# Performance work log

Hardware: AMD Instinct MI355X
Metric: run time of the kernel (lower is better)

## Reference

```python
import jax, jax.numpy as jnp
import numpy as np

N_STATE = 32  # SSM states per channel (S4D)


def lrelu(x):
    return jnp.where(x >= 0, x, 0.3 * x)


def conv1d(x, w, b, stride=1, pad=0, dil=1):
    # x: [B,C,L], w: [O,I,K]
    y = jax.lax.conv_general_dilated(
        x, w, (stride,), [(pad, pad)], rhs_dilation=(dil,),
        dimension_numbers=('NCH', 'OIH', 'NCH'))
    return y + b[None, :, None]


def batchnorm(x, g, b, eps=1e-5):
    # training-mode BatchNorm1d: stats over (B, L) per channel
    m = jnp.mean(x, axis=(0, 2), keepdims=True)
    v = jnp.var(x, axis=(0, 2), keepdims=True)
    return (x - m) * jax.lax.rsqrt(v + eps) * g[None, :, None] + b[None, :, None]


def s4_layer(u, log_dt, C2, D):
    # Diagonal S4 (S4D-Lin): u [B,H,L] -> y [B,H,L]; causal FFT conv + skip
    H, N = C2.shape[0], C2.shape[1]
    L = u.shape[-1]
    A = -0.5 + 1j * jnp.pi * jnp.arange(N, dtype=jnp.float32)            # [N]
    dtA = jnp.exp(log_dt)[:, None] * A[None, :]                          # [H,N]
    C = (C2[..., 0] + 1j * C2[..., 1]) * (jnp.exp(dtA) - 1.0) / A        # [H,N]
    vand = jnp.exp(dtA[:, :, None] * jnp.arange(L, dtype=jnp.float32))   # [H,N,L]
    K = 2.0 * jnp.real(jnp.einsum('hn,hnl->hl', C, vand))                # [H,L]
    uf = jnp.fft.rfft(u, n=2 * L)
    Kf = jnp.fft.rfft(K, n=2 * L)
    y = jnp.fft.irfft(uf * Kf[None], n=2 * L)[..., :L]
    return y + D[None, :, None] * u


def down_block(x, s4p, convs, g, b):
    # dilated residual inception down block: S4 then 4 stride-4 dilated convs
    x = s4_layer(x, *s4p)
    d1 = batchnorm(conv1d(x, convs[0][0], convs[0][1], 4, 1, 1), g, b)
    d2 = batchnorm(lrelu(conv1d(x, convs[1][0], convs[1][1], 4, 2, 2)), g, b)
    d3 = batchnorm(lrelu(conv1d(x, convs[2][0], convs[2][1], 4, 4, 4)), g, b)
    d4 = batchnorm(lrelu(conv1d(x, convs[3][0], convs[3][1], 4, 8, 8)), g, b)
    return jnp.concatenate([d1, d2, d3, d4], axis=1)


def setup_inputs() -> dict:
    key = jax.random.key(0)
    ks = iter(jax.random.split(key, 64))

    def nrm(shape, scale=1.0):
        return jax.random.normal(next(ks), shape, jnp.float32) * scale

    def logdt(H):
        lo, hi = np.log(0.001), np.log(0.1)
        return jax.random.uniform(next(ks), (H,), jnp.float32) * (hi - lo) + lo

    B, L, DIN = 16, 8192, 2
    inp = {}
    inp['x'] = nrm((B, L, DIN))
    inp['enc_w'] = nrm((64, DIN, 1), (1.0 / DIN) ** 0.5)
    inp['enc_b'] = jnp.zeros((64,), jnp.float32)
    for pfx, H in (('s4a', 64), ('s4b', 256), ('s4c', 1024)):
        inp[pfx + '_log_dt'] = logdt(H)
        inp[pfx + '_C'] = nrm((H, N_STATE, 2), 0.5 ** 0.5)
        inp[pfx + '_D'] = nrm((H,))
    for blk, C in (('b1', 64), ('b2', 256)):
        sc = (1.0 / (C * 3)) ** 0.5
        for i in range(1, 5):
            inp[f'{blk}_w{i}'] = nrm((C, C, 3), sc)
            inp[f'{blk}_b{i}'] = nrm((C,), 0.02)
    inp['bn1_g'] = jnp.ones((64,), jnp.float32)
    inp['bn1_b'] = jnp.zeros((64,), jnp.float32)
    inp['bn2_g'] = jnp.ones((256,), jnp.float32)
    inp['bn2_b'] = jnp.zeros((256,), jnp.float32)
    inp['dec1_w'] = nrm((256, 1024, 1), (1.0 / 1024) ** 0.5)
    inp['dec1_b'] = jnp.zeros((256,), jnp.float32)
    inp['dec2_w'] = nrm((1, 256, 1), (1.0 / 256) ** 0.5)
    inp['dec2_b'] = jnp.zeros((1,), jnp.float32)
    return inp


def reference(x, enc_w, enc_b,
              s4a_log_dt, s4a_C, s4a_D,
              b1_w1, b1_b1, b1_w2, b1_b2, b1_w3, b1_b3, b1_w4, b1_b4, bn1_g, bn1_b,
              s4b_log_dt, s4b_C, s4b_D,
              b2_w1, b2_b1, b2_w2, b2_b2, b2_w3, b2_b3, b2_w4, b2_b4, bn2_g, bn2_b,
              s4c_log_dt, s4c_C, s4c_D,
              dec1_w, dec1_b, dec2_w, dec2_b):
    h = conv1d(jnp.transpose(x, (0, 2, 1)), enc_w, enc_b)                 # [B,64,L]
    x1 = down_block(h, (s4a_log_dt, s4a_C, s4a_D),
                    [(b1_w1, b1_b1), (b1_w2, b1_b2), (b1_w3, b1_b3), (b1_w4, b1_b4)],
                    bn1_g, bn1_b)                                          # [B,256,L/4]
    x2 = down_block(x1, (s4b_log_dt, s4b_C, s4b_D),
                    [(b2_w1, b2_b1), (b2_w2, b2_b2), (b2_w3, b2_b3), (b2_w4, b2_b4)],
                    bn2_g, bn2_b)                                          # [B,1024,L/16]
    x3 = s4_layer(x2, s4c_log_dt, s4c_C, s4c_D)
    y = conv1d(conv1d(x3, dec1_w, dec1_b), dec2_w, dec2_b)                 # [B,1,L/16]
    ff = jnp.squeeze(y, axis=1)                                            # [B,L/16]
    return ff[..., -1:]                                                    # [B,1]
```

## Files before the change

### kernel.cpp

```cpp
#include <hip/hip_runtime.h>
#include <math.h>

#define PI_F 3.14159265358979323846f

typedef __attribute__((ext_vector_type(8))) short short8;
typedef __attribute__((ext_vector_type(4))) float f32x4;

__device__ __forceinline__ unsigned short f2bf(float f) {
    unsigned int u = __float_as_uint(f);
    unsigned int r = (u + 0x7fffu + ((u >> 16) & 1u)) >> 16;
    return (unsigned short)r;
}
__device__ __forceinline__ float bf2f(unsigned short v) {
    return __uint_as_float((unsigned int)v << 16);
}

__global__ __launch_bounds__(256) void enc_kernel(
    const float* __restrict__ x, const float* __restrict__ ew,
    const float* __restrict__ eb, unsigned short* __restrict__ u1)
{
    int idx = blockIdx.x * 256 + threadIdx.x;
    int t4 = idx & 2047;
    int b  = (idx >> 11) & 15;
    int h  = idx >> 15;
    float w0 = ew[2*h], w1 = ew[2*h+1], bb = eb[h];
    const float* xp = x + ((size_t)b*8192 + (size_t)t4*4)*2;
    float4 a = *(const float4*)xp;
    float4 c = *(const float4*)(xp + 4);
    ushort4 o;
    o.x = f2bf(fmaf(w0, a.x, fmaf(w1, a.y, bb)));
    o.y = f2bf(fmaf(w0, a.z, fmaf(w1, a.w, bb)));
    o.z = f2bf(fmaf(w0, c.x, fmaf(w1, c.y, bb)));
    o.w = f2bf(fmaf(w0, c.z, fmaf(w1, c.w, bb)));
    *(ushort4*)(u1 + ((size_t)h*16 + b)*8192 + (size_t)t4*4) = o;
}

__global__ __launch_bounds__(256) void prep_w(
    const float* __restrict__ w0, const float* __restrict__ w1,
    const float* __restrict__ w2, const float* __restrict__ w3,
    const float* __restrict__ w4, const float* __restrict__ w5,
    const float* __restrict__ w6, const float* __restrict__ w7,
    unsigned short* __restrict__ wprep)
{
    int id = blockIdx.y;
    const float* src; int Cin; size_t doff;
    switch (id) {
        case 0: src = w0; Cin = 64;  doff = 0;      break;
        case 1: src = w1; Cin = 64;  doff = 12288;  break;
        case 2: src = w2; Cin = 64;  doff = 24576;  break;
        case 3: src = w3; Cin = 64;  doff = 36864;  break;
        case 4: src = w4; Cin = 256; doff = 49152;  break;
        case 5: src = w5; Cin = 256; doff = 245760; break;
        case 6: src = w6; Cin = 256; doff = 442368; break;
        default: src = w7; Cin = 256; doff = 638976; break;
    }
    int e = blockIdx.x * 256 + threadIdx.x;
    if (e >= Cin * Cin * 3) return;
    int kb  = e / (Cin * 32);
    int rem = e - kb * (Cin * 32);
    int o   = rem >> 5;
    int kk  = rem & 31;
    int cch = kb / 6, t6 = kb % 6, k = t6 >> 1, chalf = t6 & 1;
    int c = cch * 64 + chalf * 32 + kk;
    wprep[doff + e] = f2bf(src[((size_t)o * Cin + c) * 3 + k]);
}

__global__ __launch_bounds__(128) void prep_s4(
    const float* __restrict__ log_dt, const float* __restrict__ C2,
    const float* __restrict__ Dv,
    unsigned short* __restrict__ TA, unsigned short* __restrict__ VA,
    float* __restrict__ rs, float* __restrict__ Vrs)
{
    int h = blockIdx.x, t = threadIdx.x;
    __shared__ float cn[64];
    __shared__ float sK[128];
    __shared__ unsigned short s_w[128 * 66];
    float dt = expf(log_dt[h]);
    if (t < 32) {
        int n = t;
        float e = expf(-0.5f*dt);
        float s_, c_; sincosf(PI_F*dt*n, &s_, &c_);
        float wr = e*c_, wi = e*s_;
        float ar = -0.5f, ai = PI_F*n;
        float den = 1.f/(ar*ar + ai*ai);
        float tr = wr - 1.f, ti = wi;
        float qr = (tr*ar + ti*ai)*den;
        float qi = (ti*ar - tr*ai)*den;
        float c2r = C2[((size_t)h*32+n)*2], c2i = C2[((size_t)h*32+n)*2+1];
        cn[2*n]   = 2.f*(c2r*qr - c2i*qi);
        cn[2*n+1] = 2.f*(c2r*qi + c2i*qr);
        float e128 = expf(-64.f*dt);
        float s2, c2v; sincosf(PI_F*dt*n*128.f, &s2, &c2v);
        float pr = 1.f - e128*c2v, pim = -e128*s2;
        float dr = 1.f - wr, di = -wi;
        float dd = 1.f/(dr*dr + di*di);
        Vrs[(size_t)h*64 + 2*n]   = (pr*dr + pim*di)*dd;
        Vrs[(size_t)h*64 + 2*n+1] = (pim*dr - pr*di)*dd;
    }
    __syncthreads();
    {
        float em = expf(-0.5f*dt*t);
        float Kt = 0.f;
        for (int n = 0; n < 32; n++) {
            float s_, c_; sincosf(PI_F*dt*(float)(n*t), &s_, &c_);
            Kt += cn[2*n]*em*c_ - cn[2*n+1]*em*s_;
        }
        sK[t] = Kt + (t == 0 ? Dv[h] : 0.f);
    }
    if (t < 64) {
        int n = t >> 1, ri = t & 1;
        float e = expf(-0.5f*dt);
        float s_, c_; sincosf(PI_F*dt*n, &s_, &c_);
        float wr = e*c_, wi = e*s_;
        float crn = cn[2*n], cin = cn[2*n+1];
        float pr = wr, pim = wi;
        for (int m = 0; m < 128; m++) {
            float re = crn*pr - cin*pim;
            float im = crn*pim + cin*pr;
            s_w[m*66 + t] = f2bf(ri ? -im : re);
            float nr = pr*wr - pim*wi;
            float ni = pr*wi + pim*wr;
            pr = nr; pim = ni;
        }
    } else {
        int r = t - 64; int n = r >> 1, ri = r & 1;
        float e = expf(-0.5f*dt);
        float s_, c_; sincosf(PI_F*dt*n, &s_, &c_);
        float wr = e*c_, wi = e*s_;
        float cr2 = 1.f, ci2 = 0.f;
        for (int kb = 3; kb >= 0; kb--) {
            unsigned short buf[32];
            for (int kk = 31; kk >= 0; kk--) {
                buf[kk] = f2bf(ri ? ci2 : cr2);
                float nr = cr2*wr - ci2*wi;
                float ni = cr2*wi + ci2*wr;
                cr2 = nr; ci2 = ni;
            }
            uint4* dst = (uint4*)&VA[(((size_t)h*4 + kb)*64 + r)*32];
            uint4* src = (uint4*)buf;
            dst[0]=src[0]; dst[1]=src[1]; dst[2]=src[2]; dst[3]=src[3];
        }
    }
    __syncthreads();
    {
        float acc = 0.f;
        for (int tau = 0; tau <= t; tau++) acc += sK[tau];
        rs[(size_t)h*128 + t] = acc;
    }
    for (int kb = 0; kb < 4; kb++) {
        unsigned short tb[32];
#pragma unroll
        for (int kk = 0; kk < 32; kk++) {
            int col = kb*32 + kk;
            tb[kk] = f2bf((col <= t) ? sK[t - col] : 0.f);
        }
        uint4* dst = (uint4*)&TA[(((size_t)h*6 + kb)*128 + t)*32];
        uint4* src = (uint4*)tb;
        dst[0]=src[0]; dst[1]=src[1]; dst[2]=src[2]; dst[3]=src[3];
    }
    for (int i = t; i < 1024; i += 128) {
        int kb = i >> 9;
        int rem = i & 511;
        int m = rem >> 2, kkg = rem & 3;
        *(uint4*)&TA[(((size_t)h*6 + 4 + kb)*128 + m)*32 + kkg*8] =
            *(const uint4*)&s_w[m*66 + kb*32 + kkg*8];
    }
}

template<int NCH, int LOGNCH>
__global__ __launch_bounds__(64) void s4ab_fused(
    const unsigned short* __restrict__ u, const unsigned short* __restrict__ VA,
    const float* __restrict__ Vrs, const float* __restrict__ sc,
    const float* __restrict__ sh, const float* __restrict__ log_dt,
    unsigned short* __restrict__ Sini)
{
    const int L = NCH * 128;
    __shared__ float sE[NCH * 68];
    int b = blockIdx.x, h = blockIdx.y;
    int lane = threadIdx.x;
    int nl = lane & 15, g = lane >> 4;
    float scv = sc ? sc[h] : 1.f;
    float shv = sh ? sh[h] : 0.f;

#pragma unroll
    for (int cg = 0; cg < NCH/16; cg++) {
        int c = cg*16 + nl;
        const unsigned short* up = u + ((size_t)h*16 + b)*L + c*128;
        f32x4 acc[4];
#pragma unroll
        for (int mt = 0; mt < 4; mt++) acc[mt] = (f32x4){0.f,0.f,0.f,0.f};
#pragma unroll
        for (int kb = 0; kb < 4; kb++) {
            short8 bf = *(const short8*)(up + kb*32 + g*8);
#pragma unroll
            for (int mt = 0; mt < 4; mt++) {
                short8 af = *(const short8*)(VA + (((size_t)h*4 + kb)*64 + mt*16 + nl)*32 + g*8);
                acc[mt] = __builtin_amdgcn_mfma_f32_16x16x32_bf16(af, bf, acc[mt], 0, 0, 0);
            }
        }
#pragma unroll
        for (int mt = 0; mt < 4; mt++) {
            int j0 = mt*16 + g*4;
            float4 vr = *(const float4*)(Vrs + (size_t)h*64 + j0);
            sE[c*68 + j0 + 0] = fmaf(scv, acc[mt][0], shv*vr.x);
            sE[c*68 + j0 + 1] = fmaf(scv, acc[mt][1], shv*vr.y);
            sE[c*68 + j0 + 2] = fmaf(scv, acc[mt][2], shv*vr.z);
            sE[c*68 + j0 + 3] = fmaf(scv, acc[mt][3], shv*vr.w);
        }
    }
    __syncthreads();
    if (lane < 32) {
        int n = lane;
        float dt = expf(log_dt[h]);
        float e = expf(-0.5f * dt);
        float s_, c_; sincosf(PI_F * dt * n, &s_, &c_);
        float Wr = e*c_, Wi = e*s_;
#pragma unroll
        for (int i = 0; i < 7; i++) { float r = Wr*Wr - Wi*Wi; float im = 2.f*Wr*Wi; Wr = r; Wi = im; }
        float Sr = 0.f, Si = 0.f;
        for (int c2 = 0; c2 < NCH; c2++) {
            float* ep = &sE[c2*68 + 2*n];
            float er = ep[0], ei = ep[1];
            ep[0] = Sr; ep[1] = Si;
            float r  = fmaf(Wr, Sr, fmaf(-Wi, Si, er));
            float im = fmaf(Wi, Sr, fmaf( Wr, Si, ei));
            Sr = r; Si = im;
        }
    }
    __syncthreads();
    unsigned short* sp = Sini + ((size_t)h*16 + b)*NCH*64;
    for (int i = lane*4; i < NCH*64; i += 256) {
        int c2 = i >> 6, j = i & 63;
        ushort4 q;
        q.x = f2bf(sE[c2*68 + j]);
        q.y = f2bf(sE[c2*68 + j+1]);
        q.z = f2bf(sE[c2*68 + j+2]);
        q.w = f2bf(sE[c2*68 + j+3]);
        *(ushort4*)&sp[i] = q;
    }
}

template<int NCH, int LOGNCH>
__global__ __launch_bounds__(256) void s4_gemm_c(
    const unsigned short* __restrict__ u, const unsigned short* __restrict__ Sini,
    const unsigned short* __restrict__ TA, const float* __restrict__ rs,
    const float* __restrict__ sc, const float* __restrict__ sh,
    unsigned short* __restrict__ yout)
{
    const int L = NCH * 128;
    __shared__ unsigned short s_u[64*200];
    __shared__ unsigned short s_s[64*72];
    int h = blockIdx.y;
    int tid = threadIdx.x;
    int lane = tid & 63, wid = tid >> 6;
    int nl = lane & 15, g = lane >> 4;
    int col0 = blockIdx.x * 64;
    for (int i = tid; i < 1024; i += 256) {
        int cl = i >> 4, o = i & 15;
        int col = col0 + cl; int b = col >> LOGNCH, c = col & (NCH - 1);
        *(uint4*)&s_u[cl*200 + o*8] =
            *(const uint4*)&u[((size_t)h*16 + b)*L + c*128 + o*8];
    }
    for (int i = tid; i < 1024; i += 256) {
        int cl = i >> 4, o = i & 15;
        int col = col0 + cl; int b = col >> LOGNCH, c = col & (NCH - 1);
        *(ushort4*)&s_s[cl*72 + o*4] =
            *(const ushort4*)&Sini[(((size_t)h*16 + b)*NCH + c)*64 + o*4];
    }
    __syncthreads();
    f32x4 accT[2][4], accW[2][4];
#pragma unroll
    for (int a = 0; a < 2; a++)
#pragma unroll
        for (int j = 0; j < 4; j++) { accT[a][j] = (f32x4){0,0,0,0}; accW[a][j] = (f32x4){0,0,0,0}; }
#pragma unroll
    for (int kb = 0; kb < 4; kb++) {
        short8 bfr[4];
#pragma unroll
        for (int j = 0; j < 4; j++)
            bfr[j] = *(const short8*)&s_u[(j*16 + nl)*200 + kb*32 + g*8];
#pragma unroll
        for (int mt2 = 0; mt2 < 2; mt2++) {
            int mtile = wid*2 + mt2;
            short8 af = *(const short8*)&TA[(((size_t)h*6 + kb)*128 + mtile*16 + nl)*32 + g*8];
#pragma unroll
            for (int j = 0; j < 4; j++)
                accT[mt2][j] = __builtin_amdgcn_mfma_f32_16x16x32_bf16(af, bfr[j], accT[mt2][j], 0, 0, 0);
        }
    }
#pragma unroll
    for (int kw = 0; kw < 2; kw++) {
        short8 bfr[4];
#pragma unroll
        for (int j = 0; j < 4; j++)
            bfr[j] = *(const short8*)&s_s[(j*16 + nl)*72 + kw*32 + g*8];
#pragma unroll
        for (int mt2 = 0; mt2 < 2; mt2++) {
            int mtile = wid*2 + mt2;
            short8 af = *(const short8*)&TA[(((size_t)h*6 + 4 + kw)*128 + mtile*16 + nl)*32 + g*8];
#pragma unroll
            for (int j = 0; j < 4; j++)
                accW[mt2][j] = __builtin_amdgcn_mfma_f32_16x16x32_bf16(af, bfr[j], accW[mt2][j], 0, 0, 0);
        }
    }
    float scv = sc ? sc[h] : 1.f;
    float shv = sh ? sh[h] : 0.f;
#pragma unroll
    for (int mt2 = 0; mt2 < 2; mt2++) {
        int m0 = (wid*2 + mt2)*16 + g*4;
        float4 rsv = *(const float4*)&rs[(size_t)h*128 + m0];
#pragma unroll
        for (int j = 0; j < 4; j++) {
            int col = col0 + j*16 + nl; int b = col >> LOGNCH, c = col & (NCH - 1);
            ushort4 q;
            q.x = f2bf(fmaf(scv, accT[mt2][j][0], shv*rsv.x) + accW[mt2][j][0]);
            q.y = f2bf(fmaf(scv, accT[mt2][j][1], shv*rsv.y) + accW[mt2][j][1]);
            q.z = f2bf(fmaf(scv, accT[mt2][j][2], shv*rsv.z) + accW[mt2][j][2]);
            q.w = f2bf(fmaf(scv, accT[mt2][j][3], shv*rsv.w) + accW[mt2][j][3]);
            *(ushort4*)&yout[((size_t)h*16 + b)*L + c*128 + m0] = q;
        }
    }
}

template<int CIN, int TBLK>
__global__ __launch_bounds__(256, 2) void conv_mfma4(
    const unsigned short* __restrict__ u, const unsigned short* __restrict__ wp,
    const float* __restrict__ bs0, const float* __restrict__ bs1,
    const float* __restrict__ bs2, const float* __restrict__ bs3,
    unsigned short* __restrict__ out, int Lin, int Lout)
{
    constexpr int F     = TBLK / 16;
    constexpr int NPOS  = TBLK * 4 + 16;
    constexpr int Q     = NPOS / 4;
    constexpr int NITEM = (NPOS / 8) * 64;
    constexpr int NLD   = (NITEM + 255) / 256;
    constexpr int NCC   = CIN / 64;
    constexpr int NBUF  = (NCC > 1) ? 2 : 1;
    constexpr int BUFSZ = 4 * Q * 64;
    __shared__ unsigned short s_in[NBUF * BUFSZ];

    int tid = threadIdx.x;
    int lane = tid & 63, wid = tid >> 6;
    int nl = lane & 15, g = lane >> 4;
    int t0 = blockIdx.x * TBLK;
    int b  = blockIdx.y;
    int og = blockIdx.z * 64;
    const int P0 = t0 * 4 - 8;
    const int DIL = 1 << wid;

    f32x4 acc[4][F];
#pragma unroll
    for (int m = 0; m < 4; m++)
#pragma unroll
        for (int f = 0; f < F; f++) acc[m][f] = (f32x4){0.f,0.f,0.f,0.f};

    uint4 stg[NLD];

    auto stage_load = [&](int ccbase) {
#pragma unroll
        for (int j = 0; j < NLD; j++) {
            int i = tid + 256 * j;
            uint4 v; v.x = 0u; v.y = 0u; v.z = 0u; v.w = 0u;
            if (i < NITEM) {
                int ch = i & 63, po = i >> 6;
                int p = P0 + po * 8;
                const unsigned short* gp = u + ((size_t)(ccbase + ch)*16 + b)*Lin;
                if (p >= 0 && p + 8 <= Lin) {
                    v = *(const uint4*)(gp + p);
                } else {
                    alignas(16) unsigned short t8[8];
#pragma unroll
                    for (int j2 = 0; j2 < 8; j2++) {
                        int pj = p + j2;
                        t8[j2] = ((unsigned)pj < (unsigned)Lin) ? gp[pj] : (unsigned short)0;
                    }
                    v = *(const uint4*)t8;
                }
            }
            stg[j] = v;
        }
    };
    auto stage_write = [&](int bufidx) {
        unsigned short* sb = s_in + bufidx * BUFSZ;
#pragma unroll
        for (int j = 0; j < NLD; j++) {
            int i = tid + 256 * j;
            if (i < NITEM) {
                int ch = i & 63, po = i >> 6;
                alignas(16) unsigned short t8[8];
                *(uint4*)t8 = stg[j];
#pragma unroll
                for (int jj = 0; jj < 8; jj++) {
                    int pl = po * 8 + jj;
                    int row = (pl & 3) * Q + (pl >> 2);
                    sb[row * 64 + (ch ^ ((row & 7) << 3))] = t8[jj];
                }
            }
        }
    };

    stage_load(0);
    stage_write(0);
    __syncthreads();

#pragma unroll
    for (int cc = 0; cc < NCC; cc++) {
        if (cc + 1 < NCC) stage_load((cc + 1) * 64);
        const unsigned short* sb = s_in + (NBUF > 1 ? (cc & 1) * BUFSZ : 0);
#pragma unroll
        for (int k = 0; k < 3; ++k) {
            const int off = (k - 1) * DIL + 8;
            const int r = off & 3, s = off >> 2;
#pragma unroll
            for (int chalf = 0; chalf < 2; ++chalf) {
                int kb = cc * 6 + k * 2 + chalf;
                short8 bfr[F];
#pragma unroll
                for (int f = 0; f < F; ++f) {
                    int q = f*16 + nl + s;
                    int row = r * Q + q;
                    bfr[f] = *(const short8*)&sb[row * 64 +
                        ((((chalf << 2) | g) ^ (row & 7)) << 3)];
                }
#pragma unroll
                for (int m = 0; m < 4; ++m) {
                    short8 afrag = *(const short8*)&wp[(size_t)wid*(3*CIN*CIN) +
                        ((size_t)kb*CIN + og + m*16 + nl)*32 + g*8];
#pragma unroll
                    for (int f = 0; f < F; ++f)
                        acc[m][f] = __builtin_amdgcn_mfma_f32_16x16x32_bf16(afrag, bfr[f], acc[m][f], 0, 0, 0);
                }
            }
        }
        if (cc + 1 < NCC) {
            __syncthreads();
            stage_write((cc + 1) & 1);
            __syncthreads();
        }
    }

    const float* bp = (wid == 0) ? bs0 : (wid == 1) ? bs1 : (wid == 2) ? bs2 : bs3;
#pragma unroll
    for (int m = 0; m < 4; ++m) {
#pragma unroll
        for (int f = 0; f < F; ++f) {
            int t = t0 + f*16 + nl;
#pragma unroll
            for (int r2 = 0; r2 < 4; ++r2) {
                int o = og + m*16 + g*4 + r2;
                float v = acc[m][f][r2] + bp[o];
                if (wid) v = v >= 0.f ? v : 0.3f*v;
                out[((size_t)(wid*CIN + o)*16 + b)*Lout + t] = f2bf(v);
            }
        }
    }
}

__global__ __launch_bounds__(256) void bn_stats(
    const unsigned short* __restrict__ x, const float* __restrict__ g,
    const float* __restrict__ bb, float* __restrict__ sc, float* __restrict__ sh,
    int n, int gmask)
{
    int ch = blockIdx.x;
    const unsigned short* xp = x + (size_t)ch * n;
    float s1 = 0.f, s2 = 0.f;
    for (int i = threadIdx.x*8; i < n; i += 2048) {
        uint4 raw = *(const uint4*)(xp + i);
        unsigned short us[8]; *(uint4*)us = raw;
#pragma unroll
        for (int j = 0; j < 8; j++) {
            float v = bf2f(us[j]);
            s1 += v; s2 += v*v;
        }
    }
    for (int o = 32; o > 0; o >>= 1) { s1 += __shfl_down(s1, o); s2 += __shfl_down(s2, o); }
    __shared__ float p1[4], p2[4];
    int wid = threadIdx.x >> 6;
    if ((threadIdx.x & 63) == 0) { p1[wid] = s1; p2[wid] = s2; }
    __syncthreads();
    if (threadIdx.x == 0) {
        s1 = p1[0] + p1[1] + p1[2] + p1[3];
        s2 = p2[0] + p2[1] + p2[2] + p2[3];
        float m = s1 / n;
        float var = s2 / n - m*m;
        float rstd = rsqrtf(var + 1e-5f);
        float scale = g[ch & gmask] * rstd;
        sc[ch] = scale;
        sh[ch] = fmaf(-m, scale, bb[ch & gmask]);
    }
}

__global__ __launch_bounds__(64) void s4c_all(
    const unsigned short* __restrict__ u,
    const float* __restrict__ sc, const float* __restrict__ sh,
    const float* __restrict__ log_dt, const float* __restrict__ C2,
    const float* __restrict__ Dv, float* __restrict__ x3last)
{
    __shared__ float sE[64 * 68];
    __shared__ float red[16 * 33];
    __shared__ unsigned short sVA[4 * 64 * 32];
    __shared__ alignas(16) float sVrs[64];
    int h = blockIdx.x;
    int lane = threadIdx.x;
    int nl = lane & 15, g = lane >> 4;
    float scv = sc[h], shv = sh[h];
    float dt = expf(log_dt[h]);

    {
        int t = lane, n = t >> 1, ri = t & 1;
        float e = expf(-0.5f*dt);
        float s_, c_; sincosf(PI_F*dt*n, &s_, &c_);
        float wr = e*c_, wi = e*s_;
        float cr2 = 1.f, ci2 = 0.f;
        int key = (t >> 1) & 3;
        for (int kb = 3; kb >= 0; kb--) {
            alignas(16) unsigned short buf[32];
            for (int kk = 31; kk >= 0; kk--) {
                buf[kk] = f2bf(ri ? ci2 : cr2);
                float nr = cr2*wr - ci2*wi;
                float ni = cr2*wi + ci2*wr;
                cr2 = nr; ci2 = ni;
            }
            uint4* dst = (uint4*)&sVA[(kb*64 + t)*32];
            uint4* src4 = (uint4*)buf;
#pragma unroll
            for (int cc = 0; cc < 4; cc++) dst[cc ^ key] = src4[cc];
        }
        if (ri == 0) {
            float e128 = expf(-64.f*dt);
            float s2, c2v; sincosf(PI_F*dt*n*128.f, &s2, &c2v);
            float pr = 1.f - e128*c2v, pim = -e128*s2;
            float dr = 1.f - wr, di = -wi;
            float dd = 1.f/(dr*dr + di*di);
            sVrs[2*n]   = (pr*dr + pim*di)*dd;
            sVrs[2*n+1] = (pim*dr - pr*di)*dd;
        }
    }
    __syncthreads();

    int rkey = (nl >> 1) & 3;
    for (int cg = 0; cg < 4; cg++) {
        int col = cg*16 + nl;
        int b = col >> 2, c = col & 3;
        const unsigned short* up = u + ((size_t)h*16 + b)*512 + c*128;
        f32x4 acc[4];
#pragma unroll
        for (int mt = 0; mt < 4; mt++) acc[mt] = (f32x4){0.f,0.f,0.f,0.f};
#pragma unroll
        for (int kb = 0; kb < 4; kb++) {
            short8 bf = *(const short8*)(up + kb*32 + g*8);
#pragma unroll
            for (int mt = 0; mt < 4; mt++) {
                short8 af = *(const short8*)&sVA[(kb*64 + mt*16 + nl)*32 + ((g ^ rkey) << 3)];
                acc[mt] = __builtin_amdgcn_mfma_f32_16x16x32_bf16(af, bf, acc[mt], 0, 0, 0);
            }
        }
#pragma unroll
        for (int mt = 0; mt < 4; mt++) {
            int j0 = mt*16 + g*4;
            float4 vr = *(const float4*)&sVrs[j0];
            sE[col*68 + j0 + 0] = fmaf(scv, acc[mt][0], shv*vr.x);
            sE[col*68 + j0 + 1] = fmaf(scv, acc[mt][1], shv*vr.y);
            sE[col*68 + j0 + 2] = fmaf(scv, acc[mt][2], shv*vr.z);
            sE[col*68 + j0 + 3] = fmaf(scv, acc[mt][3], shv*vr.w);
        }
    }
    __syncthreads();

    int n = lane >> 1, bh = lane & 1;
    float e = expf(-0.5f * dt);
    float s_, c_; sincosf(PI_F * dt * n, &s_, &c_);
    float wr = e*c_, wi = e*s_;
    float ar = -0.5f, ai = PI_F * n;
    float den = 1.f / (ar*ar + ai*ai);
    float tr = wr - 1.f, ti = wi;
    float qr = (tr*ar + ti*ai) * den;
    float qi = (ti*ar - tr*ai) * den;
    float c2r = C2[((size_t)h*32 + n)*2], c2i = C2[((size_t)h*32 + n)*2 + 1];
    float crv = c2r*qr - c2i*qi, civ = c2r*qi + c2i*qr;
    float Wr = wr, Wi = wi;
#pragma unroll
    for (int i = 0; i < 7; i++) { float r = Wr*Wr - Wi*Wi; float im = 2.f*Wr*Wi; Wr = r; Wi = im; }
#pragma unroll
    for (int b2 = 0; b2 < 8; b2++) {
        int b = bh*8 + b2;
        float Sr = 0.f, Si = 0.f;
#pragma unroll
        for (int c = 0; c < 4; c++) {
            int col = b*4 + c;
            float er = sE[col*68 + 2*n], ei = sE[col*68 + 2*n + 1];
            float r  = fmaf(Wr, Sr, fmaf(-Wi, Si, er));
            float im = fmaf(Wi, Sr, fmaf( Wr, Si, ei));
            Sr = r; Si = im;
        }
        red[b*33 + n] = crv*Sr - civ*Si;
    }
    __syncthreads();
    if (lane < 16) {
        int b = lane;
        float s = 0.f;
        for (int n2 = 0; n2 < 32; n2++) s += red[b*33 + n2];
        float uv = fmaf(scv, bf2f(u[((size_t)h*16 + b)*512 + 511]), shv);
        x3last[b*1024 + h] = 2.f*s + Dv[h]*uv;
    }
}

__global__ __launch_bounds__(256) void dec_kernel(
    const float* __restrict__ x3last, const float* __restrict__ w1, const float* __restrict__ b1,
    const float* __restrict__ w2, const float* __restrict__ b2, float* __restrict__ out)
{
    __shared__ float xs[1024];
    int b = blockIdx.x, tid = threadIdx.x;
    for (int i = tid; i < 1024; i += 256) xs[i] = x3last[b*1024 + i];
    __syncthreads();
    float z = b1[tid];
    const float* wpt = w1 + (size_t)tid*1024;
    for (int i = 0; i < 1024; i += 4) {
        float4 wv = *(const float4*)(wpt + i);
        z = fmaf(wv.x, xs[i],   z);
        z = fmaf(wv.y, xs[i+1], z);
        z = fmaf(wv.z, xs[i+2], z);
        z = fmaf(wv.w, xs[i+3], z);
    }
    float v = w2[tid] * z;
    for (int o = 32; o > 0; o >>= 1) v += __shfl_down(v, o);
    __shared__ float ps[4];
    if ((tid & 63) == 0) ps[tid >> 6] = v;
    __syncthreads();
    if (tid == 0) out[b] = ps[0] + ps[1] + ps[2] + ps[3] + b2[0];
}

extern "C" void kernel_launch(void* const* d_in, const int* in_sizes, int n_in,
                              void* d_out, int out_size, void* d_ws, size_t ws_size,
                              hipStream_t stream)
{
    const float* x       = (const float*)d_in[0];
    const float* enc_w   = (const float*)d_in[1];
    const float* enc_b   = (const float*)d_in[2];
    const float* s4a_ldt = (const float*)d_in[3];
    const float* s4a_C   = (const float*)d_in[4];
    const float* s4a_D   = (const float*)d_in[5];
    const float* s4b_ldt = (const float*)d_in[6];
    const float* s4b_C   = (const float*)d_in[7];
    const float* s4b_D   = (const float*)d_in[8];
    const float* s4c_ldt = (const float*)d_in[9];
    const float* s4c_C   = (const float*)d_in[10];
    const float* s4c_D   = (const float*)d_in[11];
    const float* b1w[4] = {(const float*)d_in[12], (const float*)d_in[14], (const float*)d_in[16], (const float*)d_in[18]};
    const float* b1b[4] = {(const float*)d_in[13], (const float*)d_in[15], (const float*)d_in[17], (const float*)d_in[19]};
    const float* b2w[4] = {(const float*)d_in[20], (const float*)d_in[22], (const float*)d_in[24], (const float*)d_in[26]};
    const float* b2b[4] = {(const float*)d_in[21], (const float*)d_in[23], (const float*)d_in[25], (const float*)d_in[27]};
    const float* bn1_g  = (const float*)d_in[28];
    const float* bn1_b  = (const float*)d_in[29];
    const float* bn2_g  = (const float*)d_in[30];
    const float* bn2_b  = (const float*)d_in[31];
    const float* dec1_w = (const float*)d_in[32];
    const float* dec1_b = (const float*)d_in[33];
    const float* dec2_w = (const float*)d_in[34];
    const float* dec2_b = (const float*)d_in[35];
    float* out = (float*)d_out;

    char* ws = (char*)d_ws;
    unsigned short* u1    = (unsigned short*)(ws);
    unsigned short* u3    = u1;
    unsigned short* ya    = (unsigned short*)(ws + 16777216);
    unsigned short* yb    = ya;
    unsigned short* u2    = (unsigned short*)(ws + 33554432);
    unsigned short* Sini  = (unsigned short*)(ws + 67108864);
    unsigned short* wprep = (unsigned short*)(ws + 88080384);
    unsigned short* TA_a  = (unsigned short*)(ws + 89751552);
    unsigned short* TA_b  = (unsigned short*)(ws + 92897280);
    unsigned short* VA_a  = (unsigned short*)(ws + 105480192);
    unsigned short* VA_b  = (unsigned short*)(ws + 106528768);
    float*          rs_a  = (float*)(ws + 110723072);
    float*          rs_b  = (float*)(ws + 110755840);
    float*          Vrs_a = (float*)(ws + 110886912);
    float*          Vrs_b = (float*)(ws + 110903296);
    float*          smallp= (float*)(ws + 110968832);
    float* sc1 = smallp;
    float* sh1 = smallp + 256;
    float* sc2 = smallp + 512;
    float* sh2 = smallp + 1536;
    float* x3l = smallp + 2560;

    prep_w<<<dim3(768, 8), 256, 0, stream>>>(b1w[0], b1w[1], b1w[2], b1w[3],
                                             b2w[0], b2w[1], b2w[2], b2w[3], wprep);
    prep_s4<<<64, 128, 0, stream>>>(s4a_ldt, s4a_C, s4a_D, TA_a, VA_a, rs_a, Vrs_a);
    prep_s4<<<256, 128, 0, stream>>>(s4b_ldt, s4b_C, s4b_D, TA_b, VA_b, rs_b, Vrs_b);

    enc_kernel<<<8192, 256, 0, stream>>>(x, enc_w, enc_b, u1);

    s4ab_fused<64,6><<<dim3(16, 64), 64, 0, stream>>>(u1, VA_a, Vrs_a, nullptr, nullptr, s4a_ldt, Sini);
    s4_gemm_c<64,6><<<dim3(16, 64), 256, 0, stream>>>(u1, Sini, TA_a, rs_a, nullptr, nullptr, ya);

    conv_mfma4<64,32><<<dim3(64, 16, 1), 256, 0, stream>>>(
        ya, wprep, b1b[0], b1b[1], b1b[2], b1b[3], u2, 8192, 2048);
    bn_stats<<<256, 256, 0, stream>>>(u2, bn1_g, bn1_b, sc1, sh1, 16*2048, 63);

    s4ab_fused<16,4><<<dim3(16, 256), 64, 0, stream>>>(u2, VA_b, Vrs_b, sc1, sh1, s4b_ldt, Sini);
    s4_gemm_c<16,4><<<dim3(4, 256), 256, 0, stream>>>(u2, Sini, TA_b, rs_b, sc1, sh1, yb);

    conv_mfma4<256,64><<<dim3(8, 16, 4), 256, 0, stream>>>(
        yb, wprep + 49152, b2b[0], b2b[1], b2b[2], b2b[3], u3, 2048, 512);
    bn_stats<<<1024, 256, 0, stream>>>(u3, bn2_g, bn2_b, sc2, sh2, 16*512, 255);

    s4c_all<<<1024, 64, 0, stream>>>(u3, sc2, sh2, s4c_ldt, s4c_C, s4c_D, x3l);

    dec_kernel<<<16, 256, 0, stream>>>(x3l, dec1_w, dec1_b, dec2_w, dec2_b, out);
}
```

Before: 342.2 us.

## Fuse S4 chunk-state scan and chunked GEMM into one kernel per layer

Merges the per-chunk state computation (MFMA projection plus sequential scan over chunks) and the chunked output GEMM into a single kernel. The input tile is loaded to shared memory once and reused by both phases, and the chunk-initial states stay in shared memory. This removes the Sini global round trip and one launch per S4 layer. For the first layer each block covers exactly one batch, so the scan stays serial over 64 chunks with only 32 active threads while the rest of the block waits, and shared memory use per block grows.

```diff
diff --git a/kernel.cpp b/kernel.cpp
--- a/kernel.cpp
+++ b/kernel.cpp
@@ -168,30 +168,41 @@
 }
 
 template<int NCH, int LOGNCH>
-__global__ __launch_bounds__(64) void s4ab_fused(
+__global__ __launch_bounds__(256) void s4_layer_fused(
     const unsigned short* __restrict__ u, const unsigned short* __restrict__ VA,
-    const float* __restrict__ Vrs, const float* __restrict__ sc,
+    const float* __restrict__ Vrs, const unsigned short* __restrict__ TA,
+    const float* __restrict__ rs, const float* __restrict__ sc,
     const float* __restrict__ sh, const float* __restrict__ log_dt,
-    unsigned short* __restrict__ Sini)
+    unsigned short* __restrict__ yout)
 {
     const int L = NCH * 128;
-    __shared__ float sE[NCH * 68];
-    int b = blockIdx.x, h = blockIdx.y;
-    int lane = threadIdx.x;
+    __shared__ unsigned short s_u[64*200];
+    __shared__ unsigned short s_s[64*72];
+    __shared__ float sE[64*68];
+    int h = blockIdx.y;
+    int tid = threadIdx.x;
+    int lane = tid & 63, wid = tid >> 6;
     int nl = lane & 15, g = lane >> 4;
+    int col0 = blockIdx.x * 64;
     float scv = sc ? sc[h] : 1.f;
     float shv = sh ? sh[h] : 0.f;
 
-#pragma unroll
-    for (int cg = 0; cg < NCH/16; cg++) {
-        int c = cg*16 + nl;
-        const unsigned short* up = u + ((size_t)h*16 + b)*L + c*128;
+    for (int i = tid; i < 1024; i += 256) {
+        int cl = i >> 4, o = i & 15;
+        int col = col0 + cl; int b = col >> LOGNCH, c = col & (NCH - 1);
+        *(uint4*)&s_u[cl*200 + o*8] =
+            *(const uint4*)&u[((size_t)h*16 + b)*L + c*128 + o*8];
+    }
+    __syncthreads();
+
+    {
+        int cl = wid*16 + nl;
         f32x4 acc[4];
 #pragma unroll
         for (int mt = 0; mt < 4; mt++) acc[mt] = (f32x4){0.f,0.f,0.f,0.f};
 #pragma unroll
         for (int kb = 0; kb < 4; kb++) {
-            short8 bf = *(const short8*)(up + kb*32 + g*8);
+            short8 bf = *(const short8*)&s_u[cl*200 + kb*32 + g*8];
 #pragma unroll
             for (int mt = 0; mt < 4; mt++) {
                 short8 af = *(const short8*)(VA + (((size_t)h*4 + kb)*64 + mt*16 + nl)*32 + g*8);
@@ -202,15 +213,17 @@
         for (int mt = 0; mt < 4; mt++) {
             int j0 = mt*16 + g*4;
             float4 vr = *(const float4*)(Vrs + (size_t)h*64 + j0);
-            sE[c*68 + j0 + 0] = fmaf(scv, acc[mt][0], shv*vr.x);
-            sE[c*68 + j0 + 1] = fmaf(scv, acc[mt][1], shv*vr.y);
-            sE[c*68 + j0 + 2] = fmaf(scv, acc[mt][2], shv*vr.z);
-            sE[c*68 + j0 + 3] = fmaf(scv, acc[mt][3], shv*vr.w);
-        }
-    }
-    __syncthreads();
-    if (lane < 32) {
-        int n = lane;
+            sE[cl*68 + j0 + 0] = fmaf(scv, acc[mt][0], shv*vr.x);
+            sE[cl*68 + j0 + 1] = fmaf(scv, acc[mt][1], shv*vr.y);
+            sE[cl*68 + j0 + 2] = fmaf(scv, acc[mt][2], shv*vr.z);
+            sE[cl*68 + j0 + 3] = fmaf(scv, acc[mt][3], shv*vr.w);
+        }
+    }
+    __syncthreads();
+
+    constexpr int NB = 64 / NCH;
+    if (tid < NB * 32) {
+        int bl = tid >> 5, n = tid & 31;
         float dt = expf(log_dt[h]);
         float e = expf(-0.5f * dt);
         float s_, c_; sincosf(PI_F * dt * n, &s_, &c_);
@@ -219,7 +232,7 @@
         for (int i = 0; i < 7; i++) { float r = Wr*Wr - Wi*Wi; float im = 2.f*Wr*Wi; Wr = r; Wi = im; }
         float Sr = 0.f, Si = 0.f;
         for (int c2 = 0; c2 < NCH; c2++) {
-            float* ep = &sE[c2*68 + 2*n];
+            float* ep = &sE[(bl*NCH + c2)*68 + 2*n];
             float er = ep[0], ei = ep[1];
             ep[0] = Sr; ep[1] = Si;
             float r  = fmaf(Wr, Sr, fmaf(-Wi, Si, er));
@@ -228,46 +241,18 @@
         }
     }
     __syncthreads();
-    unsigned short* sp = Sini + ((size_t)h*16 + b)*NCH*64;
-    for (int i = lane*4; i < NCH*64; i += 256) {
-        int c2 = i >> 6, j = i & 63;
+
+    for (int i = tid*4; i < 4096; i += 1024) {
+        int cl = i >> 6, j = i & 63;
         ushort4 q;
-        q.x = f2bf(sE[c2*68 + j]);
-        q.y = f2bf(sE[c2*68 + j+1]);
-        q.z = f2bf(sE[c2*68 + j+2]);
-        q.w = f2bf(sE[c2*68 + j+3]);
-        *(ushort4*)&sp[i] = q;
-    }
-}
-
-template<int NCH, int LOGNCH>
-__global__ __launch_bounds__(256) void s4_gemm_c(
-    const unsigned short* __restrict__ u, const unsigned short* __restrict__ Sini,
-    const unsigned short* __restrict__ TA, const float* __restrict__ rs,
-    const float* __restrict__ sc, const float* __restrict__ sh,
-    unsigned short* __restrict__ yout)
-{
-    const int L = NCH * 128;
-    __shared__ unsigned short s_u[64*200];
-    __shared__ unsigned short s_s[64*72];
-    int h = blockIdx.y;
-    int tid = threadIdx.x;
-    int lane = tid & 63, wid = tid >> 6;
-    int nl = lane & 15, g = lane >> 4;
-    int col0 = blockIdx.x * 64;
-    for (int i = tid; i < 1024; i += 256) {
-        int cl = i >> 4, o = i & 15;
-        int col = col0 + cl; int b = col >> LOGNCH, c = col & (NCH - 1);
-        *(uint4*)&s_u[cl*200 + o*8] =
-            *(const uint4*)&u[((size_t)h*16 + b)*L + c*128 + o*8];
-    }
-    for (int i = tid; i < 1024; i += 256) {
-        int cl = i >> 4, o = i & 15;
-        int col = col0 + cl; int b = col >> LOGNCH, c = col & (NCH - 1);
-        *(ushort4*)&s_s[cl*72 + o*4] =
-            *(const ushort4*)&Sini[(((size_t)h*16 + b)*NCH + c)*64 + o*4];
-    }
-    __syncthreads();
+        q.x = f2bf(sE[cl*68 + j]);
+        q.y = f2bf(sE[cl*68 + j+1]);
+        q.z = f2bf(sE[cl*68 + j+2]);
+        q.w = f2bf(sE[cl*68 + j+3]);
+        *(ushort4*)&s_s[cl*72 + j] = q;
+    }
+    __syncthreads();
+
     f32x4 accT[2][4], accW[2][4];
 #pragma unroll
     for (int a = 0; a < 2; a++)
@@ -303,8 +288,6 @@
                 accW[mt2][j] = __builtin_amdgcn_mfma_f32_16x16x32_bf16(af, bfr[j], accW[mt2][j], 0, 0, 0);
         }
     }
-    float scv = sc ? sc[h] : 1.f;
-    float shv = sh ? sh[h] : 0.f;
 #pragma unroll
     for (int mt2 = 0; mt2 < 2; mt2++) {
         int m0 = (wid*2 + mt2)*16 + g*4;
@@ -666,7 +649,6 @@
     unsigned short* ya    = (unsigned short*)(ws + 16777216);
     unsigned short* yb    = ya;
     unsigned short* u2    = (unsigned short*)(ws + 33554432);
-    unsigned short* Sini  = (unsigned short*)(ws + 67108864);
     unsigned short* wprep = (unsigned short*)(ws + 88080384);
     unsigned short* TA_a  = (unsigned short*)(ws + 89751552);
     unsigned short* TA_b  = (unsigned short*)(ws + 92897280);
@@ -690,15 +672,15 @@
 
     enc_kernel<<<8192, 256, 0, stream>>>(x, enc_w, enc_b, u1);
 
-    s4ab_fused<64,6><<<dim3(16, 64), 64, 0, stream>>>(u1, VA_a, Vrs_a, nullptr, nullptr, s4a_ldt, Sini);
-    s4_gemm_c<64,6><<<dim3(16, 64), 256, 0, stream>>>(u1, Sini, TA_a, rs_a, nullptr, nullptr, ya);
+    s4_layer_fused<64,6><<<dim3(16, 64), 256, 0, stream>>>(
+        u1, VA_a, Vrs_a, TA_a, rs_a, nullptr, nullptr, s4a_ldt, ya);
 
     conv_mfma4<64,32><<<dim3(64, 16, 1), 256, 0, stream>>>(
         ya, wprep, b1b[0], b1b[1], b1b[2], b1b[3], u2, 8192, 2048);
     bn_stats<<<256, 256, 0, stream>>>(u2, bn1_g, bn1_b, sc1, sh1, 16*2048, 63);
 
-    s4ab_fused<16,4><<<dim3(16, 256), 64, 0, stream>>>(u2, VA_b, Vrs_b, sc1, sh1, s4b_ldt, Sini);
-    s4_gemm_c<16,4><<<dim3(4, 256), 256, 0, stream>>>(u2, Sini, TA_b, rs_b, sc1, sh1, yb);
+    s4_layer_fused<16,4><<<dim3(4, 256), 256, 0, stream>>>(
+        u2, VA_b, Vrs_b, TA_b, rs_b, sc1, sh1, s4b_ldt, yb);
 
     conv_mfma4<256,64><<<dim3(8, 16, 4), 256, 0, stream>>>(
         yb, wprep + 49152, b2b[0], b2b[1], b2b[2], b2b[3], u3, 2048, 512);
```

Result: faster. 325.7 us (-4.8%).
